# Performance work log

Measured on AMD Instinct MI355X. Metric: run time of the kernel, lower is better.

## Reference

```python
import jax, jax.numpy as jnp
import numpy as np

REGULARIZE = 1e-4  # minimum eigenvalue clamp, matches precision_pool default
N_CHILD, N_PARENT, K_DIM = 4096, 128, 16


def setup_inputs() -> dict:
    key = jax.random.key(0)
    k1, k2, k3, k4 = jax.random.split(key, 4)
    N, M, K = N_CHILD, N_PARENT, K_DIM
    mu_children = jax.random.normal(k1, (N, K), dtype=jnp.float32)
    # SPD child covariances: A A^T + I
    A = 0.3 * jax.random.normal(k2, (N, K, K), dtype=jnp.float32)
    sigma_children = A @ jnp.swapaxes(A, -1, -2) + jnp.eye(K, dtype=jnp.float32)
    weights = jax.random.uniform(k3, (N, M), dtype=jnp.float32)
    # near-identity invertible transports Omega_{alpha i}: (M, N, K, K)
    transport = 0.1 * jax.random.normal(k4, (M, N, K, K), dtype=jnp.float32) \
        + jnp.eye(K, dtype=jnp.float32)
    return {"mu_children": mu_children, "sigma_children": sigma_children,
            "weights": weights, "transport": transport}


def reference(mu_children, sigma_children, weights, transport):
    """precision_pool vmapped over M meta-agents.

    mu_children: (N, K); sigma_children: (N, K, K);
    weights: (N, M); transport: (M, N, K, K)
    Returns (mu_pooled (M, K), sigma_pooled (M, K, K)).
    """
    # Child precisions Lambda_i = Sigma_i^{-1}
    Lambda_c = jnp.linalg.inv(sigma_children)                      # (N, K, K)
    # Transported precisions Omega Lambda Omega^T: (M, N, K, K)
    Lt = jnp.einsum('mnij,njk,mnlk->mnil', transport, Lambda_c, transport)
    # Precision-weighted sum over children: Lambda_alpha = sum_i w_i Lt_i
    Lp = jnp.einsum('nm,mnij->mij', weights, Lt)                   # (M, K, K)
    Lp = 0.5 * (Lp + jnp.swapaxes(Lp, -1, -2))                     # symmetrize
    # Eigen-clamp for numerical stability, then reconstruct
    evals, evecs = jnp.linalg.eigh(Lp)
    evals = jnp.maximum(evals, REGULARIZE)
    Lp = jnp.einsum('mij,mj,mkj->mik', evecs, evals, evecs)        # (M, K, K)
    # Transported means and information vector
    mu_t = jnp.einsum('mnij,nj->mni', transport, mu_children)      # (M, N, K)
    info = jnp.einsum('nm,mnij,mnj->mi', weights, Lt, mu_t)        # (M, K)
    sigma_pooled = jnp.linalg.inv(Lp)                              # (M, K, K)
    mu_pooled = jnp.einsum('mij,mj->mi', sigma_pooled, info)       # (M, K)
    return mu_pooled, sigma_pooled
```

## Files before the change

### kernel.cpp

```cpp
#include <hip/hip_runtime.h>
#include <hip/hip_bf16.h>

#define NCH   4096
#define NPAR  128
#define KD    16
#define CHUNK 128
#define NCHUNK (NCH / CHUNK)
#define PITCH 24

typedef __attribute__((ext_vector_type(4))) float f4;
typedef __attribute__((ext_vector_type(8))) short bh8;
typedef __attribute__((ext_vector_type(4))) int   i4;
typedef __attribute__((ext_vector_type(2))) unsigned int u2;

static __device__ __forceinline__ unsigned pk2(float a, float b) {
  float2 t; t.x = a; t.y = b;
  union { __hip_bfloat162 h2; unsigned u; } cv;
  cv.h2 = __float22bfloat162_rn(t);
  return cv.u;
}
static __device__ __forceinline__ float bflo(unsigned v) { return __uint_as_float(v << 16); }
static __device__ __forceinline__ float bfhi(unsigned v) { return __uint_as_float(v & 0xFFFF0000u); }

__global__ __launch_bounds__(256) void invert_sigma(const float* __restrict__ sig,
                                                    unsigned short* __restrict__ lam) {
  __shared__ float A[16][17];
  __shared__ float B[16][17];
  const int n = blockIdx.x;
  const int t = threadIdx.x, i = t >> 4, j = t & 15;
  A[i][j] = sig[(size_t)n * 256 + t];
  B[i][j] = (i == j) ? 1.0f : 0.0f;
  __syncthreads();
  for (int k = 0; k < 16; ++k) {
    const float ip  = 1.0f / A[k][k];
    const float akj = A[k][j] * ip;
    const float bkj = B[k][j] * ip;
    const float f   = A[i][k];
    __syncthreads();
    if (i == k) { A[i][j] = akj;      B[i][j] = bkj; }
    else        { A[i][j] -= f * akj; B[i][j] -= f * bkj; }
    __syncthreads();
  }
  __hip_bfloat16 h = __float2bfloat16(B[i][j]);
  lam[(size_t)n * 256 + t] = *reinterpret_cast<unsigned short*>(&h);
}

__global__ __launch_bounds__(256) void pool_pairs(
    const float* __restrict__ transport,
    const unsigned short* __restrict__ lam,
    const float* __restrict__ mu,
    const float* __restrict__ weights,
    float* __restrict__ Lp,
    float* __restrict__ info) {
  __shared__ unsigned short sOm[4][16 * PITCH];
  __shared__ unsigned short sLm[4][16 * PITCH];
  __shared__ float sMu[CHUNK * 16];
  __shared__ float sW[CHUNK];
  __shared__ float sRedLp[4][256];
  __shared__ float sRedIn[4][16];

  const int bx = blockIdx.x;
  const int m  = bx & (NPAR - 1);
  const int c  = bx >> 7;
  const int tid = threadIdx.x;
  const int w = tid >> 6;
  const int L = tid & 63;
  const int q = L >> 4;
  const int t = L & 15;

  #pragma unroll
  for (int r = 0; r < (CHUNK * 16) / 256; ++r) {
    const int idx = r * 256 + tid;
    sMu[idx] = mu[(size_t)c * CHUNK * 16 + idx];
  }
  if (tid < CHUNK) sW[tid] = weights[(size_t)(c * CHUNK + tid) * NPAR + m];
  __syncthreads();

  const int PER_WAVE = CHUNK / 4;
  const int n0 = c * CHUNK + w * PER_WAVE;
  unsigned short* om = sOm[w];
  unsigned short* lm = sLm[w];

  const int wr_off = (L >> 2) * PITCH + (L & 3) * 4;
  const int rd_off = t * PITCH + q * 8;

  f4 accLp = {0.f, 0.f, 0.f, 0.f};
  f4 accIn = {0.f, 0.f, 0.f, 0.f};
  const f4 zf = {0.f, 0.f, 0.f, 0.f};

  const float* tbase = transport + ((size_t)m * NCH + n0) * 256;
  const unsigned short* lbase = lam + (size_t)n0 * 256;

  f4 omNext = *(const f4*)(tbase + 4 * L);
  u2 lmNext = *(const u2*)(lbase + 4 * L);

  for (int it = 0; it < PER_WAVE; ++it) {
    const f4 omv = omNext;
    const u2 lmv = lmNext;
    const int itn = (it + 1 < PER_WAVE) ? it + 1 : it;
    omNext = *(const f4*)(tbase + (size_t)itn * 256 + 4 * L);
    lmNext = *(const u2*)(lbase + (size_t)itn * 256 + 4 * L);
    const int nloc = w * PER_WAVE + it;

    u2 omp; omp.x = pk2(omv.x, omv.y); omp.y = pk2(omv.z, omv.w);
    *(u2*)(om + wr_off) = omp;
    *(u2*)(lm + wr_off) = lmv;
    __builtin_amdgcn_wave_barrier();

    i4 aOmI = {0, 0, 0, 0}, aLmI = {0, 0, 0, 0};
    if (q < 2) {
      aOmI = *(const i4*)(om + rd_off);
      aLmI = *(const i4*)(lm + rd_off);
    }
    union { i4 i; bh8 h; } cvo, cvl, cvp;
    cvo.i = aOmI; cvl.i = aLmI;

    const float* muv = sMu + nloc * 16 + (q & 1) * 8;
    const f4 mlo = *(const f4*)(muv);
    const f4 mhi = *(const f4*)(muv + 4);
    const unsigned a0 = (unsigned)aOmI.x, a1 = (unsigned)aOmI.y,
                   a2 = (unsigned)aOmI.z, a3 = (unsigned)aOmI.w;
    float p = bflo(a0) * mlo.x + bfhi(a0) * mlo.y + bflo(a1) * mlo.z + bfhi(a1) * mlo.w +
              bflo(a2) * mhi.x + bfhi(a2) * mhi.y + bflo(a3) * mhi.z + bfhi(a3) * mhi.w;
    p += __shfl_xor(p, 16, 64);
    p += __shfl_xor(p, 32, 64);

    f4 P = __builtin_amdgcn_mfma_f32_16x16x32_bf16(cvl.h, cvo.h, zf, 0, 0, 0);

    const unsigned pkLoV = pk2(P.x, P.y);
    const unsigned pkHiV = pk2(P.z, P.w);
    const int srcA = t + (q & 1) * 32;
    int w0 = __shfl((int)pkLoV, srcA, 64);
    int w1 = __shfl((int)pkHiV, srcA, 64);
    int w2 = __shfl((int)pkLoV, srcA + 16, 64);
    int w3 = __shfl((int)pkHiV, srcA + 16, 64);
    i4 bPI;
    bPI.x = (q < 2) ? w0 : 0;
    bPI.y = (q < 2) ? w1 : 0;
    bPI.z = (q < 2) ? w2 : 0;
    bPI.w = (q < 2) ? w3 : 0;
    cvp.i = bPI;

    f4 Ct = __builtin_amdgcn_mfma_f32_16x16x32_bf16(cvo.h, cvp.h, zf, 0, 0, 0);

    const float wv = sW[nloc];
    const float wmu = wv * p;
    accLp.x += wv * Ct.x;  accIn.x += wmu * Ct.x;
    accLp.y += wv * Ct.y;  accIn.y += wmu * Ct.y;
    accLp.z += wv * Ct.z;  accIn.z += wmu * Ct.z;
    accLp.w += wv * Ct.w;  accIn.w += wmu * Ct.w;
    __builtin_amdgcn_wave_barrier();
  }

  sRedLp[w][(q * 4 + 0) * 16 + t] = accLp.x;
  sRedLp[w][(q * 4 + 1) * 16 + t] = accLp.y;
  sRedLp[w][(q * 4 + 2) * 16 + t] = accLp.z;
  sRedLp[w][(q * 4 + 3) * 16 + t] = accLp.w;

  float i0 = accIn.x, i1 = accIn.y, i2 = accIn.z, i3 = accIn.w;
  #pragma unroll
  for (int off = 1; off < 16; off <<= 1) {
    i0 += __shfl_xor(i0, off, 64);
    i1 += __shfl_xor(i1, off, 64);
    i2 += __shfl_xor(i2, off, 64);
    i3 += __shfl_xor(i3, off, 64);
  }
  if (t == 0) {
    sRedIn[w][q * 4 + 0] = i0;
    sRedIn[w][q * 4 + 1] = i1;
    sRedIn[w][q * 4 + 2] = i2;
    sRedIn[w][q * 4 + 3] = i3;
  }
  __syncthreads();

  const float s = sRedLp[0][tid] + sRedLp[1][tid] + sRedLp[2][tid] + sRedLp[3][tid];
  atomicAdd(&Lp[(size_t)m * 256 + tid], s);
  if (tid < 16) {
    const float si = sRedIn[0][tid] + sRedIn[1][tid] + sRedIn[2][tid] + sRedIn[3][tid];
    atomicAdd(&info[(size_t)m * 16 + tid], si);
  }
}

__global__ __launch_bounds__(256) void finalize(const float* __restrict__ Lp,
                                                const float* __restrict__ info,
                                                float* __restrict__ out) {
  __shared__ float A[16][17];
  __shared__ float B[16][17];
  __shared__ float infoS[16];
  const int m = blockIdx.x;
  const int tid = threadIdx.x, i = tid >> 4, j = tid & 15;
  const float* Lm = Lp + (size_t)m * 256;
  A[i][j] = 0.5f * (Lm[i * 16 + j] + Lm[j * 16 + i]);
  B[i][j] = (i == j) ? 1.0f : 0.0f;
  if (tid < 16) infoS[tid] = info[(size_t)m * 16 + tid];
  __syncthreads();
  for (int k = 0; k < 16; ++k) {
    const float ip  = 1.0f / A[k][k];
    const float akj = A[k][j] * ip;
    const float bkj = B[k][j] * ip;
    const float f   = A[i][k];
    __syncthreads();
    if (i == k) { A[i][j] = akj;      B[i][j] = bkj; }
    else        { A[i][j] -= f * akj; B[i][j] -= f * bkj; }
    __syncthreads();
  }
  out[(size_t)KD * NPAR + (size_t)m * 256 + tid] = B[i][j];
  if (tid < 16) {
    float s = 0.f;
    #pragma unroll
    for (int jj = 0; jj < 16; ++jj) s += B[tid][jj] * infoS[jj];
    out[(size_t)m * 16 + tid] = s;
  }
}

extern "C" void kernel_launch(void* const* d_in, const int* in_sizes, int n_in,
                              void* d_out, int out_size, void* d_ws, size_t ws_size,
                              hipStream_t stream) {
  const float* mu_children    = (const float*)d_in[0];
  const float* sigma_children = (const float*)d_in[1];
  const float* weights        = (const float*)d_in[2];
  const float* transport      = (const float*)d_in[3];
  float* out = (float*)d_out;

  unsigned short* lam = (unsigned short*)d_ws;
  float* Lp   = (float*)((char*)d_ws + (size_t)NCH * 256 * sizeof(unsigned short));
  float* info = Lp + (size_t)NPAR * 256;

  hipMemsetAsync(Lp, 0, (size_t)(NPAR * 256 + NPAR * 16) * sizeof(float), stream);
  invert_sigma<<<NCH, 256, 0, stream>>>(sigma_children, lam);
  pool_pairs<<<NPAR * NCHUNK, 256, 0, stream>>>(transport, lam, mu_children, weights, Lp, info);
  finalize<<<NPAR, 256, 0, stream>>>(Lp, info, out);
}
```

Measured before the change: 697.8 us.

## Load MFMA operands directly from global and replace atomics with partial sums

The inverted precisions are now stored in an MFMA-fragment-friendly layout, so each lane loads its A/B operand directly from global memory. This drops the per-wave LDS staging, the wave barriers and the bf16 unpacking for the mean product, which now uses the fp32 transport values. Global atomics and the memset are replaced by per-chunk partial buffers that the finalize kernel reduces. Half the lanes now idle during the loads, and finalize reads more data serially.

```diff
diff --git a/kernel.cpp b/kernel.cpp
--- a/kernel.cpp
+++ b/kernel.cpp
@@ -6,12 +6,10 @@
 #define KD    16
 #define CHUNK 128
 #define NCHUNK (NCH / CHUNK)
-#define PITCH 24
 
 typedef __attribute__((ext_vector_type(4))) float f4;
 typedef __attribute__((ext_vector_type(8))) short bh8;
 typedef __attribute__((ext_vector_type(4))) int   i4;
-typedef __attribute__((ext_vector_type(2))) unsigned int u2;
 
 static __device__ __forceinline__ unsigned pk2(float a, float b) {
   float2 t; t.x = a; t.y = b;
@@ -19,8 +17,6 @@
   cv.h2 = __float22bfloat162_rn(t);
   return cv.u;
 }
-static __device__ __forceinline__ float bflo(unsigned v) { return __uint_as_float(v << 16); }
-static __device__ __forceinline__ float bfhi(unsigned v) { return __uint_as_float(v & 0xFFFF0000u); }
 
 __global__ __launch_bounds__(256) void invert_sigma(const float* __restrict__ sig,
                                                     unsigned short* __restrict__ lam) {
@@ -42,7 +38,8 @@
     __syncthreads();
   }
   __hip_bfloat16 h = __float2bfloat16(B[i][j]);
-  lam[(size_t)n * 256 + t] = *reinterpret_cast<unsigned short*>(&h);
+  lam[(size_t)n * 256 + ((j >> 3) * 16 + i) * 8 + (j & 7)] =
+      *reinterpret_cast<unsigned short*>(&h);
 }
 
 __global__ __launch_bounds__(256) void pool_pairs(
@@ -50,10 +47,8 @@
     const unsigned short* __restrict__ lam,
     const float* __restrict__ mu,
     const float* __restrict__ weights,
-    float* __restrict__ Lp,
-    float* __restrict__ info) {
-  __shared__ unsigned short sOm[4][16 * PITCH];
-  __shared__ unsigned short sLm[4][16 * PITCH];
+    float* __restrict__ partLp,
+    float* __restrict__ partInfo) {
   __shared__ float sMu[CHUNK * 16];
   __shared__ float sW[CHUNK];
   __shared__ float sRedLp[4][256];
@@ -78,68 +73,62 @@
 
   const int PER_WAVE = CHUNK / 4;
   const int n0 = c * CHUNK + w * PER_WAVE;
-  unsigned short* om = sOm[w];
-  unsigned short* lm = sLm[w];
-
-  const int wr_off = (L >> 2) * PITCH + (L & 3) * 4;
-  const int rd_off = t * PITCH + q * 8;
+  const float* tb = transport + ((size_t)m * NCH + n0) * 256;
+  const unsigned short* lb = lam + (size_t)n0 * 256;
+
+  const bool act = (q < 2);
+  const int oOff = t * 16 + q * 8;
+  const int lOff = L * 8;
 
   f4 accLp = {0.f, 0.f, 0.f, 0.f};
   f4 accIn = {0.f, 0.f, 0.f, 0.f};
   const f4 zf = {0.f, 0.f, 0.f, 0.f};
 
-  const float* tbase = transport + ((size_t)m * NCH + n0) * 256;
-  const unsigned short* lbase = lam + (size_t)n0 * 256;
-
-  f4 omNext = *(const f4*)(tbase + 4 * L);
-  u2 lmNext = *(const u2*)(lbase + 4 * L);
+  f4 om0 = zf, om1 = zf;
+  i4 lmv = {0, 0, 0, 0};
+  if (act) {
+    om0 = *(const f4*)(tb + oOff);
+    om1 = *(const f4*)(tb + oOff + 4);
+    lmv = *(const i4*)(lb + lOff);
+  }
 
   for (int it = 0; it < PER_WAVE; ++it) {
-    const f4 omv = omNext;
-    const u2 lmv = lmNext;
+    const f4 a0 = om0, a1 = om1;
+    const i4 lf = lmv;
     const int itn = (it + 1 < PER_WAVE) ? it + 1 : it;
-    omNext = *(const f4*)(tbase + (size_t)itn * 256 + 4 * L);
-    lmNext = *(const u2*)(lbase + (size_t)itn * 256 + 4 * L);
+    if (act) {
+      om0 = *(const f4*)(tb + (size_t)itn * 256 + oOff);
+      om1 = *(const f4*)(tb + (size_t)itn * 256 + oOff + 4);
+      lmv = *(const i4*)(lb + (size_t)itn * 256 + lOff);
+    }
     const int nloc = w * PER_WAVE + it;
-
-    u2 omp; omp.x = pk2(omv.x, omv.y); omp.y = pk2(omv.z, omv.w);
-    *(u2*)(om + wr_off) = omp;
-    *(u2*)(lm + wr_off) = lmv;
-    __builtin_amdgcn_wave_barrier();
-
-    i4 aOmI = {0, 0, 0, 0}, aLmI = {0, 0, 0, 0};
-    if (q < 2) {
-      aOmI = *(const i4*)(om + rd_off);
-      aLmI = *(const i4*)(lm + rd_off);
-    }
-    union { i4 i; bh8 h; } cvo, cvl, cvp;
-    cvo.i = aOmI; cvl.i = aLmI;
 
     const float* muv = sMu + nloc * 16 + (q & 1) * 8;
     const f4 mlo = *(const f4*)(muv);
     const f4 mhi = *(const f4*)(muv + 4);
-    const unsigned a0 = (unsigned)aOmI.x, a1 = (unsigned)aOmI.y,
-                   a2 = (unsigned)aOmI.z, a3 = (unsigned)aOmI.w;
-    float p = bflo(a0) * mlo.x + bfhi(a0) * mlo.y + bflo(a1) * mlo.z + bfhi(a1) * mlo.w +
-              bflo(a2) * mhi.x + bfhi(a2) * mhi.y + bflo(a3) * mhi.z + bfhi(a3) * mhi.w;
+    float p = a0.x * mlo.x + a0.y * mlo.y + a0.z * mlo.z + a0.w * mlo.w +
+              a1.x * mhi.x + a1.y * mhi.y + a1.z * mhi.z + a1.w * mhi.w;
     p += __shfl_xor(p, 16, 64);
     p += __shfl_xor(p, 32, 64);
+
+    union { i4 i; bh8 h; } cvo, cvl, cvp;
+    cvo.i.x = (int)pk2(a0.x, a0.y); cvo.i.y = (int)pk2(a0.z, a0.w);
+    cvo.i.z = (int)pk2(a1.x, a1.y); cvo.i.w = (int)pk2(a1.z, a1.w);
+    cvl.i = lf;
 
     f4 P = __builtin_amdgcn_mfma_f32_16x16x32_bf16(cvl.h, cvo.h, zf, 0, 0, 0);
 
     const unsigned pkLoV = pk2(P.x, P.y);
     const unsigned pkHiV = pk2(P.z, P.w);
     const int srcA = t + (q & 1) * 32;
-    int w0 = __shfl((int)pkLoV, srcA, 64);
-    int w1 = __shfl((int)pkHiV, srcA, 64);
-    int w2 = __shfl((int)pkLoV, srcA + 16, 64);
-    int w3 = __shfl((int)pkHiV, srcA + 16, 64);
-    i4 bPI;
-    bPI.x = (q < 2) ? w0 : 0;
-    bPI.y = (q < 2) ? w1 : 0;
-    bPI.z = (q < 2) ? w2 : 0;
-    bPI.w = (q < 2) ? w3 : 0;
-    cvp.i = bPI;
+    const int w0 = __shfl((int)pkLoV, srcA, 64);
+    const int w1 = __shfl((int)pkHiV, srcA, 64);
+    const int w2 = __shfl((int)pkLoV, srcA + 16, 64);
+    const int w3 = __shfl((int)pkHiV, srcA + 16, 64);
+    cvp.i.x = act ? w0 : 0;
+    cvp.i.y = act ? w1 : 0;
+    cvp.i.z = act ? w2 : 0;
+    cvp.i.w = act ? w3 : 0;
 
     f4 Ct = __builtin_amdgcn_mfma_f32_16x16x32_bf16(cvo.h, cvp.h, zf, 0, 0, 0);
 
@@ -149,7 +138,6 @@
     accLp.y += wv * Ct.y;  accIn.y += wmu * Ct.y;
     accLp.z += wv * Ct.z;  accIn.z += wmu * Ct.z;
     accLp.w += wv * Ct.w;  accIn.w += wmu * Ct.w;
-    __builtin_amdgcn_wave_barrier();
   }
 
   sRedLp[w][(q * 4 + 0) * 16 + t] = accLp.x;
@@ -174,25 +162,39 @@
   __syncthreads();
 
   const float s = sRedLp[0][tid] + sRedLp[1][tid] + sRedLp[2][tid] + sRedLp[3][tid];
-  atomicAdd(&Lp[(size_t)m * 256 + tid], s);
+  partLp[(size_t)bx * 256 + tid] = s;
   if (tid < 16) {
     const float si = sRedIn[0][tid] + sRedIn[1][tid] + sRedIn[2][tid] + sRedIn[3][tid];
-    atomicAdd(&info[(size_t)m * 16 + tid], si);
-  }
-}
-
-__global__ __launch_bounds__(256) void finalize(const float* __restrict__ Lp,
-                                                const float* __restrict__ info,
+    partInfo[(size_t)bx * 16 + tid] = si;
+  }
+}
+
+__global__ __launch_bounds__(256) void finalize(const float* __restrict__ partLp,
+                                                const float* __restrict__ partInfo,
                                                 float* __restrict__ out) {
+  __shared__ float raw[256];
   __shared__ float A[16][17];
   __shared__ float B[16][17];
   __shared__ float infoS[16];
   const int m = blockIdx.x;
   const int tid = threadIdx.x, i = tid >> 4, j = tid & 15;
-  const float* Lm = Lp + (size_t)m * 256;
-  A[i][j] = 0.5f * (Lm[i * 16 + j] + Lm[j * 16 + i]);
+
+  float a = 0.f;
+  #pragma unroll 4
+  for (int c = 0; c < NCHUNK; ++c)
+    a += partLp[((size_t)c * NPAR + m) * 256 + tid];
+  raw[tid] = a;
+  if (tid < 16) {
+    float si = 0.f;
+    #pragma unroll 4
+    for (int c = 0; c < NCHUNK; ++c)
+      si += partInfo[((size_t)c * NPAR + m) * 16 + tid];
+    infoS[tid] = si;
+  }
+  __syncthreads();
+
+  A[i][j] = 0.5f * (raw[i * 16 + j] + raw[j * 16 + i]);
   B[i][j] = (i == j) ? 1.0f : 0.0f;
-  if (tid < 16) infoS[tid] = info[(size_t)m * 16 + tid];
   __syncthreads();
   for (int k = 0; k < 16; ++k) {
     const float ip  = 1.0f / A[k][k];
@@ -223,11 +225,11 @@
   float* out = (float*)d_out;
 
   unsigned short* lam = (unsigned short*)d_ws;
-  float* Lp   = (float*)((char*)d_ws + (size_t)NCH * 256 * sizeof(unsigned short));
-  float* info = Lp + (size_t)NPAR * 256;
-
-  hipMemsetAsync(Lp, 0, (size_t)(NPAR * 256 + NPAR * 16) * sizeof(float), stream);
+  float* partLp   = (float*)((char*)d_ws + (size_t)NCH * 256 * sizeof(unsigned short));
+  float* partInfo = partLp + (size_t)NPAR * NCHUNK * 256;
+
   invert_sigma<<<NCH, 256, 0, stream>>>(sigma_children, lam);
-  pool_pairs<<<NPAR * NCHUNK, 256, 0, stream>>>(transport, lam, mu_children, weights, Lp, info);
-  finalize<<<NPAR, 256, 0, stream>>>(Lp, info, out);
-}
+  pool_pairs<<<NPAR * NCHUNK, 256, 0, stream>>>(transport, lam, mu_children,
+                                                weights, partLp, partInfo);
+  finalize<<<NPAR, 256, 0, stream>>>(partLp, partInfo, out);
+}
```

After: 702.2 us. No clear change (+0.6%).
